# Optimization experiments

Hardware: AMD Instinct MI355X
Metric: run time of the kernel (lower is better)

The kernel has to match this reference:

```python
import jax, jax.numpy as jnp
import numpy as np

N_NODES = 100000


def _gcn_norm(edge_index, num_nodes):
    # PyG GCNConv default: add self-loops, symmetric normalization.
    src, dst = edge_index[0], edge_index[1]
    loop = jnp.arange(num_nodes, dtype=src.dtype)
    src = jnp.concatenate([src, loop])
    dst = jnp.concatenate([dst, loop])
    deg = jax.ops.segment_sum(jnp.ones_like(dst, dtype=jnp.float32), dst,
                              num_segments=num_nodes)
    dinv = jnp.where(deg > 0, jax.lax.rsqrt(jnp.maximum(deg, 1.0)), 0.0)
    norm = dinv[src] * dinv[dst]  # [E + N]
    return src, dst, norm


def _gcn_layer(x, src, dst, norm, W, b, num_nodes):
    h = x @ W                              # [N, out]
    msg = h[src] * norm[:, None]           # gather + scale, [E+N, out]
    agg = jax.ops.segment_sum(msg, dst, num_segments=num_nodes)  # scatter-add
    return agg + b


def setup_inputs() -> dict:
    key = jax.random.key(0)
    ks = jax.random.split(key, 12)
    in_c, hid = 64, 128
    dims = [in_c, hid, hid // 2, hid // 4, hid // 8, 1]
    x = jax.random.normal(ks[0], (N_NODES, in_c), dtype=jnp.float32)
    edge_index = jax.random.randint(ks[1], (2, 1600000), 0, N_NODES,
                                    dtype=jnp.int64)
    inp = {"x": x, "edge_index": edge_index}
    for i in range(5):
        fan_in = dims[i]
        s = 1.0 / np.sqrt(fan_in)
        inp[f"W{i+1}"] = jax.random.uniform(ks[2 + 2 * i], (dims[i], dims[i + 1]),
                                            minval=-s, maxval=s,
                                            dtype=jnp.float32)
        inp[f"b{i+1}"] = jnp.zeros((dims[i + 1],), dtype=jnp.float32)
    return inp


def reference(x, edge_index, W1, b1, W2, b2, W3, b3, W4, b4, W5, b5):
    num_nodes = x.shape[0]
    src, dst, norm = _gcn_norm(edge_index, num_nodes)
    h = _gcn_layer(x, src, dst, norm, W1, b1, num_nodes)
    h = jax.nn.relu(h)
    h = _gcn_layer(h, src, dst, norm, W2, b2, num_nodes)
    h = jax.nn.relu(h)
    h = _gcn_layer(h, src, dst, norm, W3, b3, num_nodes)
    h = jax.nn.relu(h)
    h = _gcn_layer(h, src, dst, norm, W4, b4, num_nodes)
    h = jax.nn.relu(h)
    h = _gcn_layer(h, src, dst, norm, W5, b5, num_nodes)
    return h
```

## Files before the change

kernel.cpp:

```cpp
#include <hip/hip_runtime.h>
#include <math.h>


#define NBIN_MAX 256
#define BSHIFT 9
#define BINW 512
#define CHUNK 8192

__global__ __launch_bounds__(256) void k_hist(const int* __restrict__ dst, int E,
                                              int nbin, int* __restrict__ binCnt) {
    __shared__ int h[NBIN_MAX];
    int t = threadIdx.x;
    for (int i = t; i < nbin; i += 256) h[i] = 0;
    __syncthreads();
    for (int e = blockIdx.x * 256 + t; e < E; e += gridDim.x * 256)
        atomicAdd(&h[dst[e] >> BSHIFT], 1);
    __syncthreads();
    for (int i = t; i < nbin; i += 256)
        if (h[i]) atomicAdd(&binCnt[i], h[i]);
}

__global__ __launch_bounds__(256) void k_binscan(const int* __restrict__ binCnt,
                                                 int nbin, int* __restrict__ binBase,
                                                 int* __restrict__ binCur) {
    __shared__ int sh[256];
    int t = threadIdx.x;
    int v = (t < nbin) ? binCnt[t] : 0;
    sh[t] = v;
    __syncthreads();
    for (int d = 1; d < 256; d <<= 1) {
        int u = (t >= d) ? sh[t - d] : 0;
        __syncthreads();
        sh[t] += u;
        __syncthreads();
    }
    int ex = sh[t] - v;
    if (t < nbin) { binBase[t] = ex; binCur[t] = ex; }
    if (t == nbin - 1) binBase[nbin] = sh[t];
}

__global__ __launch_bounds__(256) void k_binfill(const int* __restrict__ src,
                                                 const int* __restrict__ dst, int E,
                                                 int nbin, int* __restrict__ binCur,
                                                 unsigned* __restrict__ tmp) {
    __shared__ int h[NBIN_MAX];
    __shared__ int res[NBIN_MAX];
    int t = threadIdx.x;
    int e0 = blockIdx.x * CHUNK;
    int e1 = min(e0 + CHUNK, E);
    for (int i = t; i < nbin; i += 256) h[i] = 0;
    __syncthreads();
    for (int e = e0 + t; e < e1; e += 256)
        atomicAdd(&h[dst[e] >> BSHIFT], 1);
    __syncthreads();
    for (int i = t; i < nbin; i += 256)
        res[i] = h[i] ? atomicAdd(&binCur[i], h[i]) : 0;
    __syncthreads();
    for (int i = t; i < nbin; i += 256) h[i] = 0;
    __syncthreads();
    for (int e = e0 + t; e < e1; e += 256) {
        int d = dst[e];
        int b = d >> BSHIFT;
        int p = res[b] + atomicAdd(&h[b], 1);
        tmp[p] = ((unsigned)src[e] << BSHIFT) | (unsigned)(d & (BINW - 1));
    }
}

__global__ __launch_bounds__(256) void k_csr(const unsigned* __restrict__ tmp,
                                             const int* __restrict__ binBase,
                                             int n, int nbin,
                                             float* __restrict__ dinv,
                                             int* __restrict__ offs,
                                             int* __restrict__ csr) {
    __shared__ int ldeg[BINW];
    __shared__ int loff[BINW];
    __shared__ int pair[256];
    int b = blockIdx.x;
    int t = threadIdx.x;
    ldeg[t] = 0; ldeg[t + 256] = 0;
    __syncthreads();
    int lo = binBase[b], hi = binBase[b + 1];
    for (int p = lo + t; p < hi; p += 256)
        atomicAdd(&ldeg[tmp[p] & (BINW - 1u)], 1);
    __syncthreads();
    int a0 = ldeg[2 * t], a1 = ldeg[2 * t + 1];
    pair[t] = a0 + a1;
    __syncthreads();
    int v = pair[t];
    for (int d = 1; d < 256; d <<= 1) {
        int u = (t >= d) ? pair[t - d] : 0;
        __syncthreads();
        pair[t] += u;
        __syncthreads();
    }
    int ex = pair[t] - v;
    loff[2 * t] = ex;
    loff[2 * t + 1] = ex + a0;
    __syncthreads();
    int v0 = b << BSHIFT;
    for (int i = t; i < BINW; i += 256) {
        int vv = v0 + i;
        if (vv < n) {
            offs[vv] = lo + loff[i];
            dinv[vv] = 1.0f / sqrtf((float)(ldeg[i] + 1));
        }
    }
    if (t == 0 && b == nbin - 1) offs[n] = hi;
    __syncthreads();
    ldeg[t] = 0; ldeg[t + 256] = 0;
    __syncthreads();
    for (int p = lo + t; p < hi; p += 256) {
        unsigned u = tmp[p];
        int d0 = (int)(u & (BINW - 1u));
        int pos = loff[d0] + atomicAdd(&ldeg[d0], 1);
        csr[lo + pos] = (int)(u >> BSHIFT);
    }
}

template <int W, bool RELU, bool BIAS, bool L1SCALE>
__global__ __launch_bounds__(256) void k_aggv(const float* __restrict__ S,
                                              const float* __restrict__ dinv,
                                              const int* __restrict__ offs,
                                              const int* __restrict__ csr,
                                              const float* __restrict__ bg,
                                              float* __restrict__ Y, int n) {
    constexpr int LPR = W / 4;
    constexpr int G = 64 / LPR;
    int lane = threadIdx.x & 63;
    int wave = threadIdx.x >> 6;
    int v = blockIdx.x * 4 + wave;
    if (v >= n) return;
    int g = lane / LPR;
    int j = lane % LPR;
    float dv = dinv[v];
    float4 acc0 = make_float4(0.f, 0.f, 0.f, 0.f);
    float4 acc1 = make_float4(0.f, 0.f, 0.f, 0.f);
    if (g == 0) {
        float4 xv = *(const float4*)&S[(size_t)v * W + j * 4];
        float sc = L1SCALE ? dv : 1.0f;
        acc0.x = xv.x * sc; acc0.y = xv.y * sc; acc0.z = xv.z * sc; acc0.w = xv.w * sc;
    }
    int e0 = offs[v], re = offs[v + 1];
    for (int eb = e0; eb < re; eb += 2 * G) {
        int ea = eb + g, ec = eb + G + g;
        if (ea < re) {
            int u = csr[ea];
            float4 a = *(const float4*)&S[(size_t)u * W + j * 4];
            float sc = L1SCALE ? dinv[u] : 1.0f;
            acc0.x += a.x * sc; acc0.y += a.y * sc; acc0.z += a.z * sc; acc0.w += a.w * sc;
        }
        if (ec < re) {
            int u = csr[ec];
            float4 a = *(const float4*)&S[(size_t)u * W + j * 4];
            float sc = L1SCALE ? dinv[u] : 1.0f;
            acc1.x += a.x * sc; acc1.y += a.y * sc; acc1.z += a.z * sc; acc1.w += a.w * sc;
        }
    }
    acc0.x += acc1.x; acc0.y += acc1.y; acc0.z += acc1.z; acc0.w += acc1.w;
#pragma unroll
    for (int d = LPR; d < 64; d <<= 1) {
        acc0.x += __shfl_xor(acc0.x, d);
        acc0.y += __shfl_xor(acc0.y, d);
        acc0.z += __shfl_xor(acc0.z, d);
        acc0.w += __shfl_xor(acc0.w, d);
    }
    if (lane < LPR) {
        float4 r;
        r.x = dv * acc0.x; r.y = dv * acc0.y; r.z = dv * acc0.z; r.w = dv * acc0.w;
        if (BIAS) {
            float4 bv = *(const float4*)&bg[j * 4];
            r.x += bv.x; r.y += bv.y; r.z += bv.z; r.w += bv.w;
        }
        if (RELU) {
            r.x = fmaxf(r.x, 0.f); r.y = fmaxf(r.y, 0.f);
            r.z = fmaxf(r.z, 0.f); r.w = fmaxf(r.w, 0.f);
        }
        *(float4*)&Y[(size_t)v * W + j * 4] = r;
    }
}

__global__ __launch_bounds__(256) void k_agg16_gemm5(const float* __restrict__ S,
                                                     const float* __restrict__ dinv,
                                                     const int* __restrict__ offs,
                                                     const int* __restrict__ csr,
                                                     const float* __restrict__ b4,
                                                     const float* __restrict__ W5,
                                                     float* __restrict__ Y, int n) {
    constexpr int W = 16, LPR = 4, G = 16;
    int lane = threadIdx.x & 63;
    int wave = threadIdx.x >> 6;
    int v = blockIdx.x * 4 + wave;
    if (v >= n) return;
    int g = lane / LPR;
    int j = lane % LPR;
    float dv = dinv[v];
    float4 acc0 = make_float4(0.f, 0.f, 0.f, 0.f);
    float4 acc1 = make_float4(0.f, 0.f, 0.f, 0.f);
    if (g == 0) acc0 = *(const float4*)&S[(size_t)v * W + j * 4];
    int e0 = offs[v], re = offs[v + 1];
    for (int eb = e0; eb < re; eb += 2 * G) {
        int ea = eb + g, ec = eb + G + g;
        if (ea < re) {
            int u = csr[ea];
            float4 a = *(const float4*)&S[(size_t)u * W + j * 4];
            acc0.x += a.x; acc0.y += a.y; acc0.z += a.z; acc0.w += a.w;
        }
        if (ec < re) {
            int u = csr[ec];
            float4 a = *(const float4*)&S[(size_t)u * W + j * 4];
            acc1.x += a.x; acc1.y += a.y; acc1.z += a.z; acc1.w += a.w;
        }
    }
    acc0.x += acc1.x; acc0.y += acc1.y; acc0.z += acc1.z; acc0.w += acc1.w;
#pragma unroll
    for (int d = LPR; d < 64; d <<= 1) {
        acc0.x += __shfl_xor(acc0.x, d);
        acc0.y += __shfl_xor(acc0.y, d);
        acc0.z += __shfl_xor(acc0.z, d);
        acc0.w += __shfl_xor(acc0.w, d);
    }
    float4 bv = *(const float4*)&b4[j * 4];
    float4 w5 = *(const float4*)&W5[j * 4];
    float hx = fmaxf(dv * acc0.x + bv.x, 0.f);
    float hy = fmaxf(dv * acc0.y + bv.y, 0.f);
    float hz = fmaxf(dv * acc0.z + bv.z, 0.f);
    float hw = fmaxf(dv * acc0.w + bv.w, 0.f);
    float p = hx * w5.x + hy * w5.y + hz * w5.z + hw * w5.w;
    p += __shfl_xor(p, 1);
    p += __shfl_xor(p, 2);
    if (lane == 0) Y[v] = p * dv;
}

__global__ __launch_bounds__(256) void k_agg1(const float* __restrict__ S,
                                              const float* __restrict__ dinv,
                                              const int* __restrict__ offs,
                                              const int* __restrict__ csr,
                                              const float* __restrict__ bg,
                                              float* __restrict__ Y, int n) {
    int v = blockIdx.x * 256 + threadIdx.x;
    if (v >= n) return;
    float sum = S[v];
    int e = offs[v], re = offs[v + 1];
    for (; e < re; ++e) sum += S[csr[e]];
    Y[v] = dinv[v] * sum + bg[0];
}

template <int IN, int OUT, int EPI>
__global__ __launch_bounds__(256) void k_gemm(const float* __restrict__ X,
                                              const float* __restrict__ Wg,
                                              const float* __restrict__ bg,
                                              const float* __restrict__ dinv,
                                              float* __restrict__ Y, int nrows) {
    constexpr int TPR = OUT / 4;
    constexpr int GROUPS = 256 / TPR;
    constexpr int ROWS = GROUPS * 2;
    __shared__ __align__(16) float Wl[IN * OUT];
    __shared__ __align__(16) float xl[ROWS * IN];
    __shared__ float bl[OUT];
    int tid = threadIdx.x;
    for (int i = tid; i < IN * OUT; i += 256) Wl[i] = Wg[i];
    if (EPI == 0)
        for (int i = tid; i < OUT; i += 256) bl[i] = bg[i];
    int base = blockIdx.x * ROWS;
    for (int i = tid; i < ROWS * IN; i += 256) {
        int r = base + i / IN;
        xl[i] = (r < nrows) ? X[(size_t)base * IN + i] : 0.0f;
    }
    __syncthreads();
    int g = tid / TPR;
    int c0 = (tid % TPR) * 4;
    int r0 = base + g * 2, r1 = r0 + 1;
    int l0 = (g * 2) * IN, l1 = l0 + IN;
    float4 acc0 = make_float4(0.f, 0.f, 0.f, 0.f);
    float4 acc1 = make_float4(0.f, 0.f, 0.f, 0.f);
#pragma unroll 8
    for (int k = 0; k < IN; ++k) {
        float4 w = *(const float4*)&Wl[k * OUT + c0];
        float a0 = xl[l0 + k], a1 = xl[l1 + k];
        acc0.x += a0 * w.x; acc0.y += a0 * w.y; acc0.z += a0 * w.z; acc0.w += a0 * w.w;
        acc1.x += a1 * w.x; acc1.y += a1 * w.y; acc1.z += a1 * w.z; acc1.w += a1 * w.w;
    }
    if (EPI == 0) {
        float bx = bl[c0], by = bl[c0 + 1], bz = bl[c0 + 2], bw = bl[c0 + 3];
        acc0.x = fmaxf(acc0.x + bx, 0.f); acc0.y = fmaxf(acc0.y + by, 0.f);
        acc0.z = fmaxf(acc0.z + bz, 0.f); acc0.w = fmaxf(acc0.w + bw, 0.f);
        acc1.x = fmaxf(acc1.x + bx, 0.f); acc1.y = fmaxf(acc1.y + by, 0.f);
        acc1.z = fmaxf(acc1.z + bz, 0.f); acc1.w = fmaxf(acc1.w + bw, 0.f);
    } else {
        if (r0 < nrows) { float d0 = dinv[r0]; acc0.x *= d0; acc0.y *= d0; acc0.z *= d0; acc0.w *= d0; }
        if (r1 < nrows) { float d1 = dinv[r1]; acc1.x *= d1; acc1.y *= d1; acc1.z *= d1; acc1.w *= d1; }
    }
    if (r0 < nrows) *(float4*)&Y[(size_t)r0 * OUT + c0] = acc0;
    if (r1 < nrows) *(float4*)&Y[(size_t)r1 * OUT + c0] = acc1;
}

extern "C" void kernel_launch(void* const* d_in, const int* in_sizes, int n_in,
                              void* d_out, int out_size, void* d_ws, size_t ws_size,
                              hipStream_t stream) {
    const float* x  = (const float*)d_in[0];
    const int*   ei = (const int*)d_in[1];
    const float* W1 = (const float*)d_in[2];  const float* b1 = (const float*)d_in[3];
    const float* W2 = (const float*)d_in[4];  const float* b2 = (const float*)d_in[5];
    const float* W3 = (const float*)d_in[6];  const float* b3 = (const float*)d_in[7];
    const float* W4 = (const float*)d_in[8];  const float* b4 = (const float*)d_in[9];
    const float* W5 = (const float*)d_in[10]; const float* b5 = (const float*)d_in[11];

    const int N = in_sizes[0] / 64;
    const int E = in_sizes[1] / 2;
    const int* src = ei;
    const int* dst = ei + E;
    const int nbin = (N + BINW - 1) / BINW;

    char* ws = (char*)d_ws;
    size_t off = 0;
    auto alloc = [&](size_t bytes) -> void* {
        void* p = ws + off;
        off = (off + bytes + 255) & ~(size_t)255;
        return p;
    };
    float* dinv    = (float*)alloc((size_t)N * 4);
    int*   offs    = (int*)alloc((size_t)(N + 1) * 4);
    int*   binCnt  = (int*)alloc((size_t)NBIN_MAX * 4);
    int*   binBase = (int*)alloc((size_t)(NBIN_MAX + 1) * 4);
    int*   binCur  = (int*)alloc((size_t)NBIN_MAX * 4);
    int*   csr     = (int*)alloc((size_t)E * 4);
    float* s5      = (float*)alloc((size_t)N * 4);
    float* A       = (float*)alloc((size_t)N * 128 * 4);
    float* B       = (float*)alloc((size_t)N * 64 * 4);
    float* C       = (float*)alloc((size_t)N * 64 * 4);
    unsigned* tmp  = (unsigned*)C;

    hipMemsetAsync(binCnt, 0, (size_t)NBIN_MAX * 4, stream);

    k_hist<<<256, 256, 0, stream>>>(dst, E, nbin, binCnt);
    k_binscan<<<1, 256, 0, stream>>>(binCnt, nbin, binBase, binCur);
    k_binfill<<<(E + CHUNK - 1) / CHUNK, 256, 0, stream>>>(src, dst, E, nbin, binCur, tmp);
    k_csr<<<nbin, 256, 0, stream>>>(tmp, binBase, N, nbin, dinv, offs, csr);

    const int gagg = (N + 3) / 4;
    k_aggv<64, false, false, true><<<gagg, 256, 0, stream>>>(x, dinv, offs, csr, nullptr, B, N);
    k_gemm<64, 128, 0><<<(N + 15) / 16, 256, 0, stream>>>(B, W1, b1, nullptr, A, N);
    k_gemm<128, 64, 1><<<(N + 31) / 32, 256, 0, stream>>>(A, W2, nullptr, dinv, B, N);
    k_aggv<64, true, true, false><<<gagg, 256, 0, stream>>>(B, dinv, offs, csr, b2, C, N);
    k_gemm<64, 32, 1><<<(N + 63) / 64, 256, 0, stream>>>(C, W3, nullptr, dinv, B, N);
    k_aggv<32, true, true, false><<<gagg, 256, 0, stream>>>(B, dinv, offs, csr, b3, A, N);
    k_gemm<32, 16, 1><<<(N + 127) / 128, 256, 0, stream>>>(A, W4, nullptr, dinv, B, N);
    k_agg16_gemm5<<<gagg, 256, 0, stream>>>(B, dinv, offs, csr, b4, W5, s5, N);
    k_agg1<<<(N + 255) / 256, 256, 0, stream>>>(s5, dinv, offs, csr, b5, (float*)d_out, N);
}
```

Baseline: 424.8 us.

## Vectorize edge binning, prescale input features, and widen GEMM row tiling

```diff
diff --git a/kernel.cpp b/kernel.cpp
--- a/kernel.cpp
+++ b/kernel.cpp
@@ -5,7 +5,7 @@
 #define NBIN_MAX 256
 #define BSHIFT 9
 #define BINW 512
-#define CHUNK 8192
+#define CHUNK 2048
 
 __global__ __launch_bounds__(256) void k_hist(const int* __restrict__ dst, int E,
                                               int nbin, int* __restrict__ binCnt) {
@@ -13,8 +13,16 @@
     int t = threadIdx.x;
     for (int i = t; i < nbin; i += 256) h[i] = 0;
     __syncthreads();
-    for (int e = blockIdx.x * 256 + t; e < E; e += gridDim.x * 256)
-        atomicAdd(&h[dst[e] >> BSHIFT], 1);
+    int e4 = (blockIdx.x * 256 + t) * 4;
+    int stride = gridDim.x * 256 * 4;
+    for (; e4 + 3 < E; e4 += stride) {
+        int4 d = *(const int4*)&dst[e4];
+        atomicAdd(&h[d.x >> BSHIFT], 1);
+        atomicAdd(&h[d.y >> BSHIFT], 1);
+        atomicAdd(&h[d.z >> BSHIFT], 1);
+        atomicAdd(&h[d.w >> BSHIFT], 1);
+    }
+    for (; e4 < E; ++e4) atomicAdd(&h[dst[e4] >> BSHIFT], 1);
     __syncthreads();
     for (int i = t; i < nbin; i += 256)
         if (h[i]) atomicAdd(&binCnt[i], h[i]);
@@ -48,9 +56,17 @@
     int t = threadIdx.x;
     int e0 = blockIdx.x * CHUNK;
     int e1 = min(e0 + CHUNK, E);
+    int vend = e0 + ((e1 - e0) & ~3);
     for (int i = t; i < nbin; i += 256) h[i] = 0;
     __syncthreads();
-    for (int e = e0 + t; e < e1; e += 256)
+    for (int e = e0 + t * 4; e < vend; e += 1024) {
+        int4 d = *(const int4*)&dst[e];
+        atomicAdd(&h[d.x >> BSHIFT], 1);
+        atomicAdd(&h[d.y >> BSHIFT], 1);
+        atomicAdd(&h[d.z >> BSHIFT], 1);
+        atomicAdd(&h[d.w >> BSHIFT], 1);
+    }
+    for (int e = vend + t; e < e1; e += 256)
         atomicAdd(&h[dst[e] >> BSHIFT], 1);
     __syncthreads();
     for (int i = t; i < nbin; i += 256)
@@ -58,7 +74,23 @@
     __syncthreads();
     for (int i = t; i < nbin; i += 256) h[i] = 0;
     __syncthreads();
-    for (int e = e0 + t; e < e1; e += 256) {
+    for (int e = e0 + t * 4; e < vend; e += 1024) {
+        int4 d = *(const int4*)&dst[e];
+        int4 s = *(const int4*)&src[e];
+        int b0 = d.x >> BSHIFT;
+        int p0 = res[b0] + atomicAdd(&h[b0], 1);
+        tmp[p0] = ((unsigned)s.x << BSHIFT) | (unsigned)(d.x & (BINW - 1));
+        int b1 = d.y >> BSHIFT;
+        int p1 = res[b1] + atomicAdd(&h[b1], 1);
+        tmp[p1] = ((unsigned)s.y << BSHIFT) | (unsigned)(d.y & (BINW - 1));
+        int b2 = d.z >> BSHIFT;
+        int p2 = res[b2] + atomicAdd(&h[b2], 1);
+        tmp[p2] = ((unsigned)s.z << BSHIFT) | (unsigned)(d.z & (BINW - 1));
+        int b3 = d.w >> BSHIFT;
+        int p3 = res[b3] + atomicAdd(&h[b3], 1);
+        tmp[p3] = ((unsigned)s.w << BSHIFT) | (unsigned)(d.w & (BINW - 1));
+    }
+    for (int e = vend + t; e < e1; e += 256) {
         int d = dst[e];
         int b = d >> BSHIFT;
         int p = res[b] + atomicAdd(&h[b], 1);
@@ -117,7 +149,19 @@
     }
 }
 
-template <int W, bool RELU, bool BIAS, bool L1SCALE>
+__global__ __launch_bounds__(256) void k_scale(const float* __restrict__ x,
+                                               const float* __restrict__ dinv,
+                                               float* __restrict__ xs, int n) {
+    int i = blockIdx.x * 256 + threadIdx.x;
+    int v = i >> 4;
+    if (v >= n) return;
+    float4 a = *(const float4*)&x[(size_t)i * 4];
+    float dv = dinv[v];
+    a.x *= dv; a.y *= dv; a.z *= dv; a.w *= dv;
+    *(float4*)&xs[(size_t)i * 4] = a;
+}
+
+template <int W, bool RELU, bool BIAS>
 __global__ __launch_bounds__(256) void k_aggv(const float* __restrict__ S,
                                               const float* __restrict__ dinv,
                                               const int* __restrict__ offs,
@@ -135,25 +179,20 @@
     float dv = dinv[v];
     float4 acc0 = make_float4(0.f, 0.f, 0.f, 0.f);
     float4 acc1 = make_float4(0.f, 0.f, 0.f, 0.f);
-    if (g == 0) {
-        float4 xv = *(const float4*)&S[(size_t)v * W + j * 4];
-        float sc = L1SCALE ? dv : 1.0f;
-        acc0.x = xv.x * sc; acc0.y = xv.y * sc; acc0.z = xv.z * sc; acc0.w = xv.w * sc;
-    }
+    if (g == 0)
+        acc0 = *(const float4*)&S[(size_t)v * W + j * 4];
     int e0 = offs[v], re = offs[v + 1];
     for (int eb = e0; eb < re; eb += 2 * G) {
         int ea = eb + g, ec = eb + G + g;
         if (ea < re) {
-            int u = csr[ea];
+            int u = __builtin_nontemporal_load(&csr[ea]);
             float4 a = *(const float4*)&S[(size_t)u * W + j * 4];
-            float sc = L1SCALE ? dinv[u] : 1.0f;
-            acc0.x += a.x * sc; acc0.y += a.y * sc; acc0.z += a.z * sc; acc0.w += a.w * sc;
+            acc0.x += a.x; acc0.y += a.y; acc0.z += a.z; acc0.w += a.w;
         }
         if (ec < re) {
-            int u = csr[ec];
+            int u = __builtin_nontemporal_load(&csr[ec]);
             float4 a = *(const float4*)&S[(size_t)u * W + j * 4];
-            float sc = L1SCALE ? dinv[u] : 1.0f;
-            acc1.x += a.x * sc; acc1.y += a.y * sc; acc1.z += a.z * sc; acc1.w += a.w * sc;
+            acc1.x += a.x; acc1.y += a.y; acc1.z += a.z; acc1.w += a.w;
         }
     }
     acc0.x += acc1.x; acc0.y += acc1.y; acc0.z += acc1.z; acc0.w += acc1.w;
@@ -245,7 +284,7 @@
     Y[v] = dinv[v] * sum + bg[0];
 }
 
-template <int IN, int OUT, int EPI>
+template <int IN, int OUT, int EPI, int NR>
 __global__ __launch_bounds__(256) void k_gemm(const float* __restrict__ X,
                                               const float* __restrict__ Wg,
                                               const float* __restrict__ bg,
@@ -253,7 +292,7 @@
                                               float* __restrict__ Y, int nrows) {
     constexpr int TPR = OUT / 4;
     constexpr int GROUPS = 256 / TPR;
-    constexpr int ROWS = GROUPS * 2;
+    constexpr int ROWS = GROUPS * NR;
     __shared__ __align__(16) float Wl[IN * OUT];
     __shared__ __align__(16) float xl[ROWS * IN];
     __shared__ float bl[OUT];
@@ -269,29 +308,35 @@
     __syncthreads();
     int g = tid / TPR;
     int c0 = (tid % TPR) * 4;
-    int r0 = base + g * 2, r1 = r0 + 1;
-    int l0 = (g * 2) * IN, l1 = l0 + IN;
-    float4 acc0 = make_float4(0.f, 0.f, 0.f, 0.f);
-    float4 acc1 = make_float4(0.f, 0.f, 0.f, 0.f);
+    float4 acc[NR];
+#pragma unroll
+    for (int r = 0; r < NR; ++r) acc[r] = make_float4(0.f, 0.f, 0.f, 0.f);
 #pragma unroll 8
     for (int k = 0; k < IN; ++k) {
         float4 w = *(const float4*)&Wl[k * OUT + c0];
-        float a0 = xl[l0 + k], a1 = xl[l1 + k];
-        acc0.x += a0 * w.x; acc0.y += a0 * w.y; acc0.z += a0 * w.z; acc0.w += a0 * w.w;
-        acc1.x += a1 * w.x; acc1.y += a1 * w.y; acc1.z += a1 * w.z; acc1.w += a1 * w.w;
-    }
-    if (EPI == 0) {
-        float bx = bl[c0], by = bl[c0 + 1], bz = bl[c0 + 2], bw = bl[c0 + 3];
-        acc0.x = fmaxf(acc0.x + bx, 0.f); acc0.y = fmaxf(acc0.y + by, 0.f);
-        acc0.z = fmaxf(acc0.z + bz, 0.f); acc0.w = fmaxf(acc0.w + bw, 0.f);
-        acc1.x = fmaxf(acc1.x + bx, 0.f); acc1.y = fmaxf(acc1.y + by, 0.f);
-        acc1.z = fmaxf(acc1.z + bz, 0.f); acc1.w = fmaxf(acc1.w + bw, 0.f);
-    } else {
-        if (r0 < nrows) { float d0 = dinv[r0]; acc0.x *= d0; acc0.y *= d0; acc0.z *= d0; acc0.w *= d0; }
-        if (r1 < nrows) { float d1 = dinv[r1]; acc1.x *= d1; acc1.y *= d1; acc1.z *= d1; acc1.w *= d1; }
-    }
-    if (r0 < nrows) *(float4*)&Y[(size_t)r0 * OUT + c0] = acc0;
-    if (r1 < nrows) *(float4*)&Y[(size_t)r1 * OUT + c0] = acc1;
+#pragma unroll
+        for (int r = 0; r < NR; ++r) {
+            float a = xl[(g * NR + r) * IN + k];
+            acc[r].x += a * w.x; acc[r].y += a * w.y;
+            acc[r].z += a * w.z; acc[r].w += a * w.w;
+        }
+    }
+#pragma unroll
+    for (int r = 0; r < NR; ++r) {
+        int row = base + g * NR + r;
+        if (row >= nrows) continue;
+        float4 o = acc[r];
+        if (EPI == 0) {
+            o.x = fmaxf(o.x + bl[c0], 0.f);
+            o.y = fmaxf(o.y + bl[c0 + 1], 0.f);
+            o.z = fmaxf(o.z + bl[c0 + 2], 0.f);
+            o.w = fmaxf(o.w + bl[c0 + 3], 0.f);
+        } else {
+            float d0 = dinv[row];
+            o.x *= d0; o.y *= d0; o.z *= d0; o.w *= d0;
+        }
+        *(float4*)&Y[(size_t)row * OUT + c0] = o;
+    }
 }
 
 extern "C" void kernel_launch(void* const* d_in, const int* in_sizes, int n_in,
@@ -329,6 +374,7 @@
     float* B       = (float*)alloc((size_t)N * 64 * 4);
     float* C       = (float*)alloc((size_t)N * 64 * 4);
     unsigned* tmp  = (unsigned*)C;
+    float* xs      = A;
 
     hipMemsetAsync(binCnt, 0, (size_t)NBIN_MAX * 4, stream);
 
@@ -338,13 +384,14 @@
     k_csr<<<nbin, 256, 0, stream>>>(tmp, binBase, N, nbin, dinv, offs, csr);
 
     const int gagg = (N + 3) / 4;
-    k_aggv<64, false, false, true><<<gagg, 256, 0, stream>>>(x, dinv, offs, csr, nullptr, B, N);
-    k_gemm<64, 128, 0><<<(N + 15) / 16, 256, 0, stream>>>(B, W1, b1, nullptr, A, N);
-    k_gemm<128, 64, 1><<<(N + 31) / 32, 256, 0, stream>>>(A, W2, nullptr, dinv, B, N);
-    k_aggv<64, true, true, false><<<gagg, 256, 0, stream>>>(B, dinv, offs, csr, b2, C, N);
-    k_gemm<64, 32, 1><<<(N + 63) / 64, 256, 0, stream>>>(C, W3, nullptr, dinv, B, N);
-    k_aggv<32, true, true, false><<<gagg, 256, 0, stream>>>(B, dinv, offs, csr, b3, A, N);
-    k_gemm<32, 16, 1><<<(N + 127) / 128, 256, 0, stream>>>(A, W4, nullptr, dinv, B, N);
+    k_scale<<<(N * 16 + 255) / 256, 256, 0, stream>>>(x, dinv, xs, N);
+    k_aggv<64, false, false><<<gagg, 256, 0, stream>>>(xs, dinv, offs, csr, nullptr, B, N);
+    k_gemm<64, 128, 0, 4><<<(N + 31) / 32, 256, 0, stream>>>(B, W1, b1, nullptr, A, N);
+    k_gemm<128, 64, 1, 2><<<(N + 31) / 32, 256, 0, stream>>>(A, W2, nullptr, dinv, B, N);
+    k_aggv<64, true, true><<<gagg, 256, 0, stream>>>(B, dinv, offs, csr, b2, C, N);
+    k_gemm<64, 32, 1, 2><<<(N + 63) / 64, 256, 0, stream>>>(C, W3, nullptr, dinv, B, N);
+    k_aggv<32, true, true><<<gagg, 256, 0, stream>>>(B, dinv, offs, csr, b3, A, N);
+    k_gemm<32, 16, 1, 2><<<(N + 127) / 128, 256, 0, stream>>>(A, W4, nullptr, dinv, B, N);
     k_agg16_gemm5<<<gagg, 256, 0, stream>>>(B, dinv, offs, csr, b4, W5, s5, N);
     k_agg1<<<(N + 255) / 256, 256, 0, stream>>>(s5, dinv, offs, csr, b5, (float*)d_out, N);
 }
```

Result: slower. 448.7 us (+5.6%).
